# Performance work log

Measured on AMD Instinct MI355X. Metric: run time of the kernel, lower is better.

## Reference

```python
import jax, jax.numpy as jnp
import numpy as np

B, S, D = 4, 2048, 1024
H = 16
HD = D // H  # 64


def setup_inputs() -> dict:
    key = jax.random.key(0)
    ks = jax.random.split(key, 6)
    scale = 1.0 / np.sqrt(D)
    return {
        "x": jax.random.normal(ks[0], (B, S, D), dtype=jnp.float32),
        "Wq": jax.random.normal(ks[1], (D, D), dtype=jnp.float32) * scale,
        "Wk": jax.random.normal(ks[2], (D, D), dtype=jnp.float32) * scale,
        "Wv": jax.random.normal(ks[3], (D, D), dtype=jnp.float32) * scale,
        "Wo": jax.random.normal(ks[4], (D, D), dtype=jnp.float32) * scale,
        "bo": jax.random.normal(ks[5], (D,), dtype=jnp.float32) * scale,
    }


def reference(x, Wq, Wk, Wv, Wo, bo):
    b, s, _ = x.shape
    q = (x @ Wq).reshape(b, s, H, HD)
    k = (x @ Wk).reshape(b, s, H, HD)
    v = (x @ Wv).reshape(b, s, H, HD)
    # scores: [b, h, q, k]
    scores = jnp.einsum("bqhd,bkhd->bhqk", q, k)
    # causal mask (upper triangle, diagonal=1, is masked out)
    causal = jnp.tril(jnp.ones((s, s), dtype=bool))
    scores = jnp.where(causal, scores, -jnp.inf)
    # NOTE: source divides by head_dim**2 (keys.shape[-1]**2), not sqrt(head_dim)
    attn = jax.nn.softmax(scores / (HD ** 2), axis=-1)
    ctx = jnp.einsum("bhqk,bkhd->bqhd", attn, v).reshape(b, s, D)
    return ctx @ Wo + bo
```

## Files before the change

### kernel.cpp

```cpp
#include <hip/hip_runtime.h>
#include <hip/hip_bf16.h>
#include <stdint.h>

typedef short          bf16x8 __attribute__((ext_vector_type(8)));
typedef float          f32x4  __attribute__((ext_vector_type(4)));
typedef float          f32x16 __attribute__((ext_vector_type(16)));
typedef unsigned short u16x8  __attribute__((ext_vector_type(8)));

#define MFMA_BF16(a, b, c) __builtin_amdgcn_mfma_f32_16x16x32_bf16((a), (b), (c), 0, 0, 0)
#define MFMA32(a, b, c)    __builtin_amdgcn_mfma_f32_32x32x16_bf16((a), (b), (c), 0, 0, 0)

__device__ __forceinline__ void gl2lds16(const void* g, void* l) {
  __builtin_amdgcn_global_load_lds((const __attribute__((address_space(1))) void*)g,
                                   (__attribute__((address_space(3))) void*)l,
                                   16, 0, 0);
}

__device__ __forceinline__ unsigned short f2bf(float f) {
  union { float f; unsigned int u; } v;
  v.f = f;
  unsigned int r = v.u + 0x7FFFu + ((v.u >> 16) & 1u);
  return (unsigned short)(r >> 16);
}

__device__ __forceinline__ unsigned int pack2tr(float lo, float hi) {
  union { float f; unsigned int u; } a, b;
  a.f = lo; b.f = hi;
  return __builtin_amdgcn_perm(b.u, a.u, 0x07060302u);
}

__global__ void k_prep(const float* __restrict__ x, unsigned short* __restrict__ xb,
                       const float* __restrict__ W0, const float* __restrict__ W1,
                       const float* __restrict__ W2, const float* __restrict__ W3,
                       unsigned short* __restrict__ T0, unsigned short* __restrict__ T1,
                       unsigned short* __restrict__ T2, unsigned short* __restrict__ T3) {
  if (blockIdx.x < 4096) {
    int i = (blockIdx.x * 256 + threadIdx.x) * 8;
    float4 a = *(const float4*)(x + i);
    float4 b = *(const float4*)(x + i + 4);
    u16x8 o;
    o[0] = f2bf(a.x); o[1] = f2bf(a.y); o[2] = f2bf(a.z); o[3] = f2bf(a.w);
    o[4] = f2bf(b.x); o[5] = f2bf(b.y); o[6] = f2bf(b.z); o[7] = f2bf(b.w);
    *(u16x8*)(xb + i) = o;
  } else {
    const int idx = blockIdx.x - 4096;
    const int z = idx >> 10, rem = idx & 1023;
    const int k0 = (rem >> 5) * 32, n0 = (rem & 31) * 32;
    const float* W = (z == 0) ? W0 : (z == 1) ? W1 : (z == 2) ? W2 : W3;
    unsigned short* T = (z == 0) ? T0 : (z == 1) ? T1 : (z == 2) ? T2 : T3;
    __shared__ float tile[32][33];
    int tx = threadIdx.x & 31, ty = threadIdx.x >> 5;
#pragma unroll
    for (int i = 0; i < 4; ++i)
      tile[ty + i * 8][tx] = W[(size_t)(k0 + ty + i * 8) * 1024 + n0 + tx];
    __syncthreads();
#pragma unroll
    for (int i = 0; i < 4; ++i)
      T[(size_t)(n0 + ty + i * 8) * 1024 + k0 + tx] = f2bf(tile[tx][ty + i * 8]);
  }
}

__global__ __launch_bounds__(256, 2)
void k_gemm_qkv(const unsigned short* __restrict__ A,
                const unsigned short* __restrict__ BtQ, const unsigned short* __restrict__ BtK,
                const unsigned short* __restrict__ BtV,
                unsigned short* __restrict__ Qb, unsigned short* __restrict__ Kb,
                unsigned short* __restrict__ Vt) {
  const int tid = threadIdx.x;
  const int w = tid >> 6, lane = tid & 63;
  const int quad = lane >> 4, t16 = lane & 15;
  const int wm = w >> 1, wn = w & 1;
  const int m0 = blockIdx.x * 128;
  const int n0 = blockIdx.y * 128;

  __shared__ unsigned short As[2][4096];
  __shared__ unsigned short Bs[2][3 * 4096];

  f32x4 acc[3][4][4];
#pragma unroll
  for (int j = 0; j < 3; ++j)
#pragma unroll
    for (int i = 0; i < 4; ++i)
#pragma unroll
      for (int n = 0; n < 4; ++n) acc[j][i][n] = (f32x4){0.f, 0.f, 0.f, 0.f};

  const int srow = lane >> 2, g4 = lane & 3;
  const int arow0 = w * 32 + srow, arow1 = arow0 + 16;
  const unsigned short* Ap0 = A + (size_t)(m0 + arow0) * 1024 + (g4 ^ ((arow0 >> 1) & 3)) * 8;
  const unsigned short* Ap1 = A + (size_t)(m0 + arow1) * 1024 + (g4 ^ ((arow1 >> 1) & 3)) * 8;
  const unsigned short* Bp[6];
  int bOff[6];
#pragma unroll
  for (int i = 0; i < 6; ++i) {
    const int c = w * 6 + i;
    const int j = c >> 3, cc = c & 7;
    const int row = cc * 16 + srow;
    const unsigned short* Bj = (j == 0) ? BtQ : (j == 1) ? BtK : BtV;
    Bp[i] = Bj + (size_t)(n0 + row) * 1024 + (g4 ^ ((row >> 1) & 3)) * 8;
    bOff[i] = j * 4096 + cc * 512;
  }

  auto loadT = [&](int kk) {
    const int bufi = kk & 1;
    const int ko = kk * 32;
    gl2lds16(Ap0 + ko, &As[bufi][w * 1024]);
    gl2lds16(Ap1 + ko, &As[bufi][w * 1024 + 512]);
#pragma unroll
    for (int i = 0; i < 6; ++i) gl2lds16(Bp[i] + ko, &Bs[bufi][bOff[i]]);
  };

  const int ga = quad ^ ((t16 >> 1) & 3);
  const int arows = wm * 64 + t16;
  const int brows = wn * 64 + t16;

  loadT(0);
  __syncthreads();

  for (int kk = 0; kk < 32; ++kk) {
    if (kk + 1 < 32) loadT(kk + 1);
    const unsigned short* Asb = As[kk & 1];
    const unsigned short* Bsb = Bs[kk & 1];
    bf16x8 af[4];
#pragma unroll
    for (int mi = 0; mi < 4; ++mi)
      af[mi] = *(const bf16x8*)&Asb[(arows + mi * 16) * 32 + ga * 8];
#pragma unroll
    for (int j = 0; j < 3; ++j)
#pragma unroll
      for (int ni = 0; ni < 4; ++ni) {
        bf16x8 bfr = *(const bf16x8*)&Bsb[j * 4096 + (brows + ni * 16) * 32 + ga * 8];
#pragma unroll
        for (int mi = 0; mi < 4; ++mi)
          acc[j][mi][ni] = MFMA_BF16(af[mi], bfr, acc[j][mi][ni]);
      }
    __syncthreads();
  }

#pragma unroll
  for (int j = 0; j < 2; ++j) {
    unsigned short* P = (j == 0) ? Qb : Kb;
#pragma unroll
    for (int mi = 0; mi < 4; ++mi) {
      const int row = m0 + wm * 64 + mi * 16 + quad * 4;
#pragma unroll
      for (int ni = 0; ni < 4; ++ni) {
        const int col = n0 + wn * 64 + ni * 16 + t16;
        f32x4 v = acc[j][mi][ni];
#pragma unroll
        for (int r = 0; r < 4; ++r) P[(size_t)(row + r) * 1024 + col] = f2bf(v[r]);
      }
    }
  }
  const int h = (n0 >> 6) + wn;
#pragma unroll
  for (int mi = 0; mi < 4; ++mi) {
    const int m = m0 + wm * 64 + mi * 16 + quad * 4;
    const int b = m >> 11, s = m & 2047;
#pragma unroll
    for (int ni = 0; ni < 4; ++ni) {
      const int d = ni * 16 + t16;
      f32x4 v = acc[2][mi][ni];
      ushort4 pv4;
      pv4.x = f2bf(v[0]); pv4.y = f2bf(v[1]); pv4.z = f2bf(v[2]); pv4.w = f2bf(v[3]);
      *(ushort4*)&Vt[(size_t)((b * 16 + h) * 64 + d) * 2048 + s] = pv4;
    }
  }
}

__global__ __launch_bounds__(256, 3)
void k_gemm_o(const unsigned short* __restrict__ A, const unsigned short* __restrict__ Bt,
              float* __restrict__ C, const float* __restrict__ bias) {
  const int tid = threadIdx.x;
  const int w = tid >> 6, lane = tid & 63;
  const int quad = lane >> 4, t16 = lane & 15;
  const int wm = w >> 1, wn = w & 1;
  const int m0 = blockIdx.x * 128;
  const int n0 = blockIdx.y * 128;

  __shared__ unsigned short As[2][4096];
  __shared__ unsigned short Bs[2][4096];

  f32x4 acc[4][4];
#pragma unroll
  for (int i = 0; i < 4; ++i)
#pragma unroll
    for (int j = 0; j < 4; ++j) acc[i][j] = (f32x4){0.f, 0.f, 0.f, 0.f};

  const int srow = lane >> 2, g4 = lane & 3;
  const int arow0 = w * 32 + srow, arow1 = arow0 + 16;
  const int ac0 = g4 ^ ((arow0 >> 1) & 3);
  const int ac1 = g4 ^ ((arow1 >> 1) & 3);
  const unsigned short* Ap0 = A + (size_t)(m0 + arow0) * 1024 + ac0 * 8;
  const unsigned short* Ap1 = A + (size_t)(m0 + arow1) * 1024 + ac1 * 8;
  const unsigned short* Bp0 = Bt + (size_t)(n0 + arow0) * 1024 + ac0 * 8;
  const unsigned short* Bp1 = Bt + (size_t)(n0 + arow1) * 1024 + ac1 * 8;

  auto loadT = [&](int kk) {
    const int bufi = kk & 1;
    const int ko = kk * 32;
    gl2lds16(Ap0 + ko, &As[bufi][w * 1024]);
    gl2lds16(Ap1 + ko, &As[bufi][w * 1024 + 512]);
    gl2lds16(Bp0 + ko, &Bs[bufi][w * 1024]);
    gl2lds16(Bp1 + ko, &Bs[bufi][w * 1024 + 512]);
  };

  const int ga = quad ^ ((t16 >> 1) & 3);
  const int arows = wm * 64 + t16;
  const int brows = wn * 64 + t16;

  loadT(0);
  __syncthreads();

  for (int kk = 0; kk < 32; ++kk) {
    if (kk + 1 < 32) loadT(kk + 1);
    const unsigned short* Asb = As[kk & 1];
    const unsigned short* Bsb = Bs[kk & 1];
    bf16x8 af[4], bfr[4];
#pragma unroll
    for (int mi = 0; mi < 4; ++mi)
      af[mi] = *(const bf16x8*)&Asb[(arows + mi * 16) * 32 + ga * 8];
#pragma unroll
    for (int ni = 0; ni < 4; ++ni)
      bfr[ni] = *(const bf16x8*)&Bsb[(brows + ni * 16) * 32 + ga * 8];
#pragma unroll
    for (int mi = 0; mi < 4; ++mi)
#pragma unroll
      for (int ni = 0; ni < 4; ++ni)
        acc[mi][ni] = MFMA_BF16(af[mi], bfr[ni], acc[mi][ni]);
    __syncthreads();
  }

#pragma unroll
  for (int mi = 0; mi < 4; ++mi) {
    const int row = m0 + wm * 64 + mi * 16 + quad * 4;
#pragma unroll
    for (int ni = 0; ni < 4; ++ni) {
      const int col = n0 + wn * 64 + ni * 16 + t16;
      const float bv = bias[col];
      f32x4 v = acc[mi][ni];
#pragma unroll
      for (int r = 0; r < 4; ++r) C[(size_t)(row + r) * 1024 + col] = v[r] + bv;
    }
  }
}

__global__ __launch_bounds__(256, 2)
void k_attn(const unsigned short* __restrict__ Q, const unsigned short* __restrict__ K,
            const unsigned short* __restrict__ Vt, unsigned short* __restrict__ ctx) {
  const int tid = threadIdx.x;
  const int w = tid >> 6, lane = tid & 63;
  const int ln31 = lane & 31, hh = lane >> 5;
  const int bh = blockIdx.x;
  const int qt = 15 - blockIdx.y;
  const int b = bh >> 4, h = bh & 15;
  const int q0 = qt * 128;

  __shared__ unsigned short Ks[2][128 * 64];
  __shared__ unsigned short Vts[2][64 * 128];
  __shared__ unsigned short Ps[4 * 32 * 64];
  unsigned short* Qs = Ps;
  unsigned short* Pw = &Ps[w * 2048];

#pragma unroll
  for (int i = 0; i < 4; ++i) {
    const int chunk = w * 4 + i;
    const int row = chunk * 8 + (lane >> 3);
    const int c = (lane & 7) ^ (row & 7);
    gl2lds16(Q + (size_t)(b * 2048 + q0 + row) * 1024 + h * 64 + c * 8, &Qs[chunk * 512]);
  }

  auto loadKV = [&](int kt) {
    const int k0 = kt * 128;
    const int bufi = kt & 1;
#pragma unroll
    for (int i = 0; i < 4; ++i) {
      const int chunk = w * 4 + i;
      const int row = chunk * 8 + (lane >> 3);
      const int c = (lane & 7) ^ (row & 7);
      gl2lds16(K + (size_t)(b * 2048 + k0 + row) * 1024 + h * 64 + c * 8,
               &Ks[bufi][chunk * 512]);
    }
#pragma unroll
    for (int i = 0; i < 4; ++i) {
      const int chunk = w * 4 + i;
      const int row = chunk * 4 + (lane >> 4);
      const int c = (lane & 15) ^ (row & 7);
      gl2lds16(Vt + (size_t)(bh * 64 + row) * 2048 + k0 + c * 8, &Vts[bufi][chunk * 512]);
    }
  };

  loadKV(0);
  __syncthreads();

  const int qq = ln31;
  bf16x8 qf[4];
#pragma unroll
  for (int t = 0; t < 4; ++t)
    qf[t] = *(const bf16x8*)&Qs[(w * 32 + qq) * 64 + ((2 * t + hh) ^ (qq & 7)) * 8];

  f32x16 kZ;
#pragma unroll
  for (int i = 0; i < 16; ++i) kZ[i] = 0.f;
  f32x16 oacc0 = kZ, oacc1 = kZ, lacc = kZ;
  bf16x8 onesB;
#pragma unroll
  for (int i = 0; i < 8; ++i) onesB[i] = (short)0x3F80;

  const float C1 = 2.44140625e-4f;
  const float C2 = 2.9802322387695312e-8f;

  const unsigned short* KsB = Ks[0];
  const unsigned short* VtsB = Vts[0];

  auto sgroup = [&](int g, bool masked) {
    f32x16 sc;
#pragma unroll
    for (int t = 0; t < 4; ++t) {
      bf16x8 kf = *(const bf16x8*)&KsB[(g * 32 + ln31) * 64 + ((2 * t + hh) ^ (ln31 & 7)) * 8];
      sc = (t == 0) ? MFMA32(kf, qf[0], kZ) : MFMA32(kf, qf[t], sc);
    }
#pragma unroll
    for (int r2 = 0; r2 < 4; ++r2) {
      float ev[4];
#pragma unroll
      for (int r = 0; r < 4; ++r) {
        const float s = sc[r2 * 4 + r];
        float e = fmaf(s, fmaf(s, C2, C1), 1.0f);
        if (masked) {
          const int krow = r + 8 * r2 + 4 * hh;
          if (krow > qq) e = 0.f;
        }
        ev[r] = e;
      }
      uint2 pp;
      pp.x = pack2tr(ev[0], ev[1]);
      pp.y = pack2tr(ev[2], ev[3]);
      *(uint2*)&Pw[qq * 64 + ((((g & 1) * 4 + r2) ^ (qq & 7)) * 8) + hh * 4] = pp;
    }
  };
  auto zgroup = [&](int g) {
    uint2 z; z.x = 0u; z.y = 0u;
#pragma unroll
    for (int r2 = 0; r2 < 4; ++r2)
      *(uint2*)&Pw[qq * 64 + ((((g & 1) * 4 + r2) ^ (qq & 7)) * 8) + hh * 4] = z;
  };
  auto pv = [&](int half) {
#pragma unroll
    for (int t = 0; t < 4; ++t) {
      bf16x8 pf = *(const bf16x8*)&Pw[qq * 64 + ((2 * t + hh) ^ (qq & 7)) * 8];
      lacc = MFMA32(pf, onesB, lacc);
      const int gv = 2 * t + hh + half * 8;
      bf16x8 vf0 = *(const bf16x8*)&VtsB[ln31 * 128 + ((gv ^ (ln31 & 7)) * 8)];
      bf16x8 vf1 = *(const bf16x8*)&VtsB[(32 + ln31) * 128 + ((gv ^ (ln31 & 7)) * 8)];
      oacc0 = MFMA32(pf, vf0, oacc0);
      oacc1 = MFMA32(pf, vf1, oacc1);
    }
  };

  const int nk = qt + 1;
  for (int kt = 0; kt < nk; ++kt) {
    if (kt + 1 < nk) loadKV(kt + 1);
    KsB = Ks[kt & 1];
    VtsB = Vts[kt & 1];

    if (kt != qt) {
      sgroup(0, false); sgroup(1, false); pv(0);
      sgroup(2, false); sgroup(3, false); pv(1);
    } else {
      if (w == 0)      { sgroup(0, true);  zgroup(1); }
      else if (w == 1) { sgroup(0, false); sgroup(1, true); }
      else             { sgroup(0, false); sgroup(1, false); }
      pv(0);
      if (w >= 2) {
        if (w == 2) { sgroup(2, true);  zgroup(3); }
        else        { sgroup(2, false); sgroup(3, true); }
        pv(1);
      }
    }
    __syncthreads();
  }

#pragma unroll
  for (int r2 = 0; r2 < 4; ++r2) {
#pragma unroll
    for (int r = 0; r < 4; ++r) {
      const int reg = r2 * 4 + r;
      const int qrow = r + 8 * r2 + 4 * hh;
      const float li = __builtin_amdgcn_rcpf(lacc[reg]);
      const size_t base = (size_t)(b * 2048 + q0 + w * 32 + qrow) * 1024 + h * 64;
      ctx[base + ln31] = f2bf(oacc0[reg] * li);
      ctx[base + 32 + ln31] = f2bf(oacc1[reg] * li);
    }
  }
}

extern "C" void kernel_launch(void* const* d_in, const int* in_sizes, int n_in,
                              void* d_out, int out_size, void* d_ws, size_t ws_size,
                              hipStream_t stream) {
  (void)in_sizes; (void)n_in; (void)out_size; (void)ws_size;
  const float* x  = (const float*)d_in[0];
  const float* Wq = (const float*)d_in[1];
  const float* Wk = (const float*)d_in[2];
  const float* Wv = (const float*)d_in[3];
  const float* Wo = (const float*)d_in[4];
  const float* bo = (const float*)d_in[5];
  float* out = (float*)d_out;

  char* ws = (char*)d_ws;
  const size_t MB = 1u << 20;
  unsigned short* xb  = (unsigned short*)(ws + 0 * MB);
  unsigned short* WqT = (unsigned short*)(ws + 16 * MB);
  unsigned short* WkT = (unsigned short*)(ws + 18 * MB);
  unsigned short* WvT = (unsigned short*)(ws + 20 * MB);
  unsigned short* WoT = (unsigned short*)(ws + 22 * MB);
  unsigned short* Qb  = (unsigned short*)(ws + 24 * MB);
  unsigned short* Kb  = (unsigned short*)(ws + 40 * MB);
  unsigned short* Vtb = (unsigned short*)(ws + 56 * MB);
  unsigned short* ctx = xb;

  k_prep<<<dim3(8192), dim3(256), 0, stream>>>(x, xb, Wq, Wk, Wv, Wo, WqT, WkT, WvT, WoT);
  k_gemm_qkv<<<dim3(64, 8), dim3(256), 0, stream>>>(xb, WqT, WkT, WvT, Qb, Kb, Vtb);
  k_attn<<<dim3(64, 16), dim3(256), 0, stream>>>(Qb, Kb, Vtb, ctx);
  k_gemm_o<<<dim3(64, 8), dim3(256), 0, stream>>>(ctx, WoT, out, bo);
}
```

Before: 232.0 us.

## Switch GEMMs to 32x32x16 MFMA and split QKV into separate per-matrix blocks

Result: slower. 245.9 us (+6.0%).

```diff
diff --git a/kernel.cpp b/kernel.cpp
--- a/kernel.cpp
+++ b/kernel.cpp
@@ -7,8 +7,7 @@
 typedef float          f32x16 __attribute__((ext_vector_type(16)));
 typedef unsigned short u16x8  __attribute__((ext_vector_type(8)));
 
-#define MFMA_BF16(a, b, c) __builtin_amdgcn_mfma_f32_16x16x32_bf16((a), (b), (c), 0, 0, 0)
-#define MFMA32(a, b, c)    __builtin_amdgcn_mfma_f32_32x32x16_bf16((a), (b), (c), 0, 0, 0)
+#define MFMA32(a, b, c) __builtin_amdgcn_mfma_f32_32x32x16_bf16((a), (b), (c), 0, 0, 0)
 
 __device__ __forceinline__ void gl2lds16(const void* g, void* l) {
   __builtin_amdgcn_global_load_lds((const __attribute__((address_space(1))) void*)g,
@@ -60,131 +59,14 @@
   }
 }
 
-__global__ __launch_bounds__(256, 2)
-void k_gemm_qkv(const unsigned short* __restrict__ A,
-                const unsigned short* __restrict__ BtQ, const unsigned short* __restrict__ BtK,
-                const unsigned short* __restrict__ BtV,
-                unsigned short* __restrict__ Qb, unsigned short* __restrict__ Kb,
-                unsigned short* __restrict__ Vt) {
-  const int tid = threadIdx.x;
-  const int w = tid >> 6, lane = tid & 63;
-  const int quad = lane >> 4, t16 = lane & 15;
+__device__ __forceinline__ void gemm_loop32(const unsigned short* __restrict__ A,
+                                            const unsigned short* __restrict__ Bt,
+                                            int m0, int n0, int w, int lane,
+                                            unsigned short (&As)[2][4096],
+                                            unsigned short (&Bs)[2][4096],
+                                            f32x16 acc[2][2]) {
+  const int ln31 = lane & 31, hh = lane >> 5;
   const int wm = w >> 1, wn = w & 1;
-  const int m0 = blockIdx.x * 128;
-  const int n0 = blockIdx.y * 128;
-
-  __shared__ unsigned short As[2][4096];
-  __shared__ unsigned short Bs[2][3 * 4096];
-
-  f32x4 acc[3][4][4];
-#pragma unroll
-  for (int j = 0; j < 3; ++j)
-#pragma unroll
-    for (int i = 0; i < 4; ++i)
-#pragma unroll
-      for (int n = 0; n < 4; ++n) acc[j][i][n] = (f32x4){0.f, 0.f, 0.f, 0.f};
-
-  const int srow = lane >> 2, g4 = lane & 3;
-  const int arow0 = w * 32 + srow, arow1 = arow0 + 16;
-  const unsigned short* Ap0 = A + (size_t)(m0 + arow0) * 1024 + (g4 ^ ((arow0 >> 1) & 3)) * 8;
-  const unsigned short* Ap1 = A + (size_t)(m0 + arow1) * 1024 + (g4 ^ ((arow1 >> 1) & 3)) * 8;
-  const unsigned short* Bp[6];
-  int bOff[6];
-#pragma unroll
-  for (int i = 0; i < 6; ++i) {
-    const int c = w * 6 + i;
-    const int j = c >> 3, cc = c & 7;
-    const int row = cc * 16 + srow;
-    const unsigned short* Bj = (j == 0) ? BtQ : (j == 1) ? BtK : BtV;
-    Bp[i] = Bj + (size_t)(n0 + row) * 1024 + (g4 ^ ((row >> 1) & 3)) * 8;
-    bOff[i] = j * 4096 + cc * 512;
-  }
-
-  auto loadT = [&](int kk) {
-    const int bufi = kk & 1;
-    const int ko = kk * 32;
-    gl2lds16(Ap0 + ko, &As[bufi][w * 1024]);
-    gl2lds16(Ap1 + ko, &As[bufi][w * 1024 + 512]);
-#pragma unroll
-    for (int i = 0; i < 6; ++i) gl2lds16(Bp[i] + ko, &Bs[bufi][bOff[i]]);
-  };
-
-  const int ga = quad ^ ((t16 >> 1) & 3);
-  const int arows = wm * 64 + t16;
-  const int brows = wn * 64 + t16;
-
-  loadT(0);
-  __syncthreads();
-
-  for (int kk = 0; kk < 32; ++kk) {
-    if (kk + 1 < 32) loadT(kk + 1);
-    const unsigned short* Asb = As[kk & 1];
-    const unsigned short* Bsb = Bs[kk & 1];
-    bf16x8 af[4];
-#pragma unroll
-    for (int mi = 0; mi < 4; ++mi)
-      af[mi] = *(const bf16x8*)&Asb[(arows + mi * 16) * 32 + ga * 8];
-#pragma unroll
-    for (int j = 0; j < 3; ++j)
-#pragma unroll
-      for (int ni = 0; ni < 4; ++ni) {
-        bf16x8 bfr = *(const bf16x8*)&Bsb[j * 4096 + (brows + ni * 16) * 32 + ga * 8];
-#pragma unroll
-        for (int mi = 0; mi < 4; ++mi)
-          acc[j][mi][ni] = MFMA_BF16(af[mi], bfr, acc[j][mi][ni]);
-      }
-    __syncthreads();
-  }
-
-#pragma unroll
-  for (int j = 0; j < 2; ++j) {
-    unsigned short* P = (j == 0) ? Qb : Kb;
-#pragma unroll
-    for (int mi = 0; mi < 4; ++mi) {
-      const int row = m0 + wm * 64 + mi * 16 + quad * 4;
-#pragma unroll
-      for (int ni = 0; ni < 4; ++ni) {
-        const int col = n0 + wn * 64 + ni * 16 + t16;
-        f32x4 v = acc[j][mi][ni];
-#pragma unroll
-        for (int r = 0; r < 4; ++r) P[(size_t)(row + r) * 1024 + col] = f2bf(v[r]);
-      }
-    }
-  }
-  const int h = (n0 >> 6) + wn;
-#pragma unroll
-  for (int mi = 0; mi < 4; ++mi) {
-    const int m = m0 + wm * 64 + mi * 16 + quad * 4;
-    const int b = m >> 11, s = m & 2047;
-#pragma unroll
-    for (int ni = 0; ni < 4; ++ni) {
-      const int d = ni * 16 + t16;
-      f32x4 v = acc[2][mi][ni];
-      ushort4 pv4;
-      pv4.x = f2bf(v[0]); pv4.y = f2bf(v[1]); pv4.z = f2bf(v[2]); pv4.w = f2bf(v[3]);
-      *(ushort4*)&Vt[(size_t)((b * 16 + h) * 64 + d) * 2048 + s] = pv4;
-    }
-  }
-}
-
-__global__ __launch_bounds__(256, 3)
-void k_gemm_o(const unsigned short* __restrict__ A, const unsigned short* __restrict__ Bt,
-              float* __restrict__ C, const float* __restrict__ bias) {
-  const int tid = threadIdx.x;
-  const int w = tid >> 6, lane = tid & 63;
-  const int quad = lane >> 4, t16 = lane & 15;
-  const int wm = w >> 1, wn = w & 1;
-  const int m0 = blockIdx.x * 128;
-  const int n0 = blockIdx.y * 128;
-
-  __shared__ unsigned short As[2][4096];
-  __shared__ unsigned short Bs[2][4096];
-
-  f32x4 acc[4][4];
-#pragma unroll
-  for (int i = 0; i < 4; ++i)
-#pragma unroll
-    for (int j = 0; j < 4; ++j) acc[i][j] = (f32x4){0.f, 0.f, 0.f, 0.f};
 
   const int srow = lane >> 2, g4 = lane & 3;
   const int arow0 = w * 32 + srow, arow1 = arow0 + 16;
@@ -204,9 +86,17 @@
     gl2lds16(Bp1 + ko, &Bs[bufi][w * 1024 + 512]);
   };
 
-  const int ga = quad ^ ((t16 >> 1) & 3);
-  const int arows = wm * 64 + t16;
-  const int brows = wn * 64 + t16;
+  const int sw0 = hh ^ ((ln31 >> 1) & 3);
+  const int sw1 = (2 + hh) ^ ((ln31 >> 1) & 3);
+  const int ar = wm * 64 + ln31;
+  const int br = wn * 64 + ln31;
+
+#pragma unroll
+  for (int mi = 0; mi < 2; ++mi)
+#pragma unroll
+    for (int ni = 0; ni < 2; ++ni)
+#pragma unroll
+      for (int r = 0; r < 16; ++r) acc[mi][ni][r] = 0.f;
 
   loadT(0);
   __syncthreads();
@@ -215,32 +105,113 @@
     if (kk + 1 < 32) loadT(kk + 1);
     const unsigned short* Asb = As[kk & 1];
     const unsigned short* Bsb = Bs[kk & 1];
-    bf16x8 af[4], bfr[4];
-#pragma unroll
-    for (int mi = 0; mi < 4; ++mi)
-      af[mi] = *(const bf16x8*)&Asb[(arows + mi * 16) * 32 + ga * 8];
-#pragma unroll
-    for (int ni = 0; ni < 4; ++ni)
-      bfr[ni] = *(const bf16x8*)&Bsb[(brows + ni * 16) * 32 + ga * 8];
-#pragma unroll
-    for (int mi = 0; mi < 4; ++mi)
-#pragma unroll
-      for (int ni = 0; ni < 4; ++ni)
-        acc[mi][ni] = MFMA_BF16(af[mi], bfr[ni], acc[mi][ni]);
+    bf16x8 af[2][2], bfr[2][2];
+#pragma unroll
+    for (int mi = 0; mi < 2; ++mi) {
+      af[mi][0] = *(const bf16x8*)&Asb[(ar + mi * 32) * 32 + sw0 * 8];
+      af[mi][1] = *(const bf16x8*)&Asb[(ar + mi * 32) * 32 + sw1 * 8];
+    }
+#pragma unroll
+    for (int ni = 0; ni < 2; ++ni) {
+      bfr[ni][0] = *(const bf16x8*)&Bsb[(br + ni * 32) * 32 + sw0 * 8];
+      bfr[ni][1] = *(const bf16x8*)&Bsb[(br + ni * 32) * 32 + sw1 * 8];
+    }
+#pragma unroll
+    for (int ks = 0; ks < 2; ++ks)
+#pragma unroll
+      for (int mi = 0; mi < 2; ++mi)
+#pragma unroll
+        for (int ni = 0; ni < 2; ++ni)
+          acc[mi][ni] = MFMA32(af[mi][ks], bfr[ni][ks], acc[mi][ni]);
     __syncthreads();
   }
-
-#pragma unroll
-  for (int mi = 0; mi < 4; ++mi) {
-    const int row = m0 + wm * 64 + mi * 16 + quad * 4;
-#pragma unroll
-    for (int ni = 0; ni < 4; ++ni) {
-      const int col = n0 + wn * 64 + ni * 16 + t16;
-      const float bv = bias[col];
-      f32x4 v = acc[mi][ni];
-#pragma unroll
-      for (int r = 0; r < 4; ++r) C[(size_t)(row + r) * 1024 + col] = v[r] + bv;
-    }
+}
+
+__global__ __launch_bounds__(256, 3)
+void k_gemm_qkv(const unsigned short* __restrict__ A,
+                const unsigned short* __restrict__ BtQ, const unsigned short* __restrict__ BtK,
+                const unsigned short* __restrict__ BtV,
+                unsigned short* __restrict__ Qb, unsigned short* __restrict__ Kb,
+                unsigned short* __restrict__ Vt) {
+  const int tid = threadIdx.x;
+  const int w = tid >> 6, lane = tid & 63;
+  const int ln31 = lane & 31, hh = lane >> 5;
+  const int wm = w >> 1, wn = w & 1;
+  const int ysel = blockIdx.y >> 3;
+  const unsigned short* Bt = (ysel == 0) ? BtQ : (ysel == 1) ? BtK : BtV;
+  const int m0 = blockIdx.x * 128;
+  const int n0 = (blockIdx.y & 7) * 128;
+
+  __shared__ unsigned short As[2][4096];
+  __shared__ unsigned short Bs[2][4096];
+  f32x16 acc[2][2];
+
+  gemm_loop32(A, Bt, m0, n0, w, lane, As, Bs, acc);
+
+  if (ysel < 2) {
+    unsigned short* P = (ysel == 0) ? Qb : Kb;
+#pragma unroll
+    for (int mi = 0; mi < 2; ++mi)
+#pragma unroll
+      for (int ni = 0; ni < 2; ++ni) {
+        const int col = n0 + wn * 64 + ni * 32 + ln31;
+#pragma unroll
+        for (int r = 0; r < 16; ++r) {
+          const int row = m0 + wm * 64 + mi * 32 + (r & 3) + 8 * (r >> 2) + 4 * hh;
+          P[(size_t)row * 1024 + col] = f2bf(acc[mi][ni][r]);
+        }
+      }
+  } else {
+    const int h = (n0 >> 6) + wn;
+#pragma unroll
+    for (int mi = 0; mi < 2; ++mi) {
+      const int mbase = m0 + wm * 64 + mi * 32 + 4 * hh;
+      const int b = mbase >> 11;
+#pragma unroll
+      for (int ni = 0; ni < 2; ++ni) {
+        const int d = ni * 32 + ln31;
+#pragma unroll
+        for (int r2 = 0; r2 < 4; ++r2) {
+          const int s = (mbase + 8 * r2) & 2047;
+          ushort4 pv4;
+          pv4.x = f2bf(acc[mi][ni][4 * r2 + 0]);
+          pv4.y = f2bf(acc[mi][ni][4 * r2 + 1]);
+          pv4.z = f2bf(acc[mi][ni][4 * r2 + 2]);
+          pv4.w = f2bf(acc[mi][ni][4 * r2 + 3]);
+          *(ushort4*)&Vt[(size_t)((b * 16 + h) * 64 + d) * 2048 + s] = pv4;
+        }
+      }
+    }
+  }
+}
+
+__global__ __launch_bounds__(256, 3)
+void k_gemm_o(const unsigned short* __restrict__ A, const unsigned short* __restrict__ Bt,
+              float* __restrict__ C, const float* __restrict__ bias) {
+  const int tid = threadIdx.x;
+  const int w = tid >> 6, lane = tid & 63;
+  const int ln31 = lane & 31, hh = lane >> 5;
+  const int wm = w >> 1, wn = w & 1;
+  const int m0 = blockIdx.x * 128;
+  const int n0 = blockIdx.y * 128;
+
+  __shared__ unsigned short As[2][4096];
+  __shared__ unsigned short Bs[2][4096];
+  f32x16 acc[2][2];
+
+  gemm_loop32(A, Bt, m0, n0, w, lane, As, Bs, acc);
+
+#pragma unroll
+  for (int ni = 0; ni < 2; ++ni) {
+    const int col = n0 + wn * 64 + ni * 32 + ln31;
+    const float bv = bias[col];
+#pragma unroll
+    for (int mi = 0; mi < 2; ++mi)
+#pragma unroll
+      for (int r = 0; r < 16; ++r) {
+        const int row = m0 + wm * 64 + mi * 32 + (r & 3) + 8 * (r >> 2) + 4 * hh;
+        C[(size_t)row * 1024 + col] = acc[mi][ni][r] + bv;
+      }
   }
 }
 
@@ -419,7 +390,7 @@
   unsigned short* ctx = xb;
 
   k_prep<<<dim3(8192), dim3(256), 0, stream>>>(x, xb, Wq, Wk, Wv, Wo, WqT, WkT, WvT, WoT);
-  k_gemm_qkv<<<dim3(64, 8), dim3(256), 0, stream>>>(xb, WqT, WkT, WvT, Qb, Kb, Vtb);
+  k_gemm_qkv<<<dim3(64, 24), dim3(256), 0, stream>>>(xb, WqT, WkT, WvT, Qb, Kb, Vtb);
   k_attn<<<dim3(64, 16), dim3(256), 0, stream>>>(Qb, Kb, Vtb, ctx);
   k_gemm_o<<<dim3(64, 8), dim3(256), 0, stream>>>(ctx, WoT, out, bo);
 }
```
